# Optimization experiments

Measured on AMD Instinct MI355X. Metric: run time of the kernel, lower is better.

## Reference

```python
import jax, jax.numpy as jnp
import numpy as np

N, E, F_IN, EDGE_DIM, EMB, H, L, DENSE = 50000, 800000, 16, 4, 32, 4, 2, 128
HC = EMB * H


def setup_inputs() -> dict:
    ks = iter(jax.random.split(jax.random.key(0), 64))

    def w(shape, fan):
        return jax.random.normal(next(ks), shape, jnp.float32) / np.float32(np.sqrt(fan))

    inp = {}
    inp['x'] = jax.random.normal(next(ks), (N, F_IN), jnp.float32)
    inp['edge_index'] = jax.random.randint(next(ks), (2, E), 0, N, jnp.int32)
    inp['edge_attr'] = jax.random.normal(next(ks), (E, EDGE_DIM), jnp.float32)
    # layer-0 TransformerConv (F_IN -> EMB, H heads) + transf Linear
    inp['Wq0'] = w((F_IN, HC), F_IN); inp['bq0'] = w((HC,), HC)
    inp['Wk0'] = w((F_IN, HC), F_IN); inp['bk0'] = w((HC,), HC)
    inp['Wv0'] = w((F_IN, HC), F_IN); inp['bv0'] = w((HC,), HC)
    inp['We0'] = w((EDGE_DIM, HC), EDGE_DIM)
    inp['Ws0'] = w((F_IN, HC), F_IN); inp['bs0'] = w((HC,), HC)
    inp['Wt0'] = w((HC, EMB), HC); inp['bt0'] = w((EMB,), EMB)
    # stacked L inner layers (EMB -> EMB)
    inp['Wq'] = w((L, EMB, HC), EMB); inp['bq'] = w((L, HC), HC)
    inp['Wk'] = w((L, EMB, HC), EMB); inp['bk'] = w((L, HC), HC)
    inp['Wv'] = w((L, EMB, HC), EMB); inp['bv'] = w((L, HC), HC)
    inp['We'] = w((L, EDGE_DIM, HC), EDGE_DIM)
    inp['Ws'] = w((L, EMB, HC), EMB); inp['bs'] = w((L, HC), HC)
    inp['Wt'] = w((L, HC, EMB), HC); inp['bt'] = w((L, EMB), EMB)
    # dense head
    inp['W1'] = w((EMB, DENSE), EMB); inp['b1'] = w((DENSE,), DENSE)
    inp['W2'] = w((DENSE, DENSE // 2), DENSE); inp['b2'] = w((DENSE // 2,), DENSE)
    inp['W3'] = w((DENSE // 2, 1), DENSE // 2); inp['b3'] = w((1,), 1)
    return inp


def _tconv(h, edge_attr, src, dst, Wq, bq, Wk, bk, Wv, bv, We, Ws, bs):
    """PyG TransformerConv: edge-conditioned multi-head attention + root skip."""
    n = h.shape[0]
    q = (h @ Wq + bq).reshape(n, H, EMB)
    k = (h @ Wk + bk).reshape(n, H, EMB)
    v = (h @ Wv + bv).reshape(n, H, EMB)
    e = (edge_attr @ We).reshape(-1, H, EMB)          # [E,H,C]
    kj = k[src] + e                                   # gather + edge bias
    logits = (q[dst] * kj).sum(-1) / np.float32(np.sqrt(EMB))  # [E,H]
    m = jax.ops.segment_max(logits, dst, num_segments=n)       # segment softmax
    p = jnp.exp(logits - m[dst])
    z = jax.ops.segment_sum(p, dst, num_segments=n)
    alpha = p / (z[dst] + 1e-16)
    msg = (v[src] + e) * alpha[:, :, None]
    out = jax.ops.segment_sum(msg, dst, num_segments=n).reshape(n, HC)
    return out + h @ Ws + bs                          # root_weight skip


def _forward(x, edge_attr, Wq0, bq0, Wk0, bk0, Wv0, bv0, We0, Ws0, bs0, Wt0, bt0,
             Wq, bq, Wk, bk, Wv, bv, We, Ws, bs, Wt, bt,
             W1, b1, W2, b2, W3, b3, edge_index):
    src, dst = edge_index[0], edge_index[1]
    h = _tconv(x, edge_attr, src, dst, Wq0, bq0, Wk0, bk0, Wv0, bv0, We0, Ws0, bs0)
    h = jax.nn.relu(h @ Wt0 + bt0)
    for i in range(L):
        h = _tconv(h, edge_attr, src, dst, Wq[i], bq[i], Wk[i], bk[i],
                   Wv[i], bv[i], We[i], Ws[i], bs[i])
        h = jax.nn.relu(h @ Wt[i] + bt[i])
    h = jax.nn.relu(h @ W1 + b1)
    h = jax.nn.relu(h @ W2 + b2)
    return jax.nn.sigmoid(h @ W3 + b3)                # [N,1]


def reference(x, edge_index, edge_attr, Wq0, bq0, Wk0, bk0, Wv0, bv0, We0, Ws0, bs0,
              Wt0, bt0, Wq, bq, Wk, bk, Wv, bv, We, Ws, bs, Wt, bt,
              W1, b1, W2, b2, W3, b3):
    return _forward(x, edge_attr, Wq0, bq0, Wk0, bk0, Wv0, bv0, We0, Ws0, bs0,
                    Wt0, bt0, Wq, bq, Wk, bk, Wv, bv, We, Ws, bs, Wt, bt,
                    W1, b1, W2, b2, W3, b3, edge_index)
```

## Files before the change

### kernel.cpp

```cpp
#include <hip/hip_runtime.h>

#define NN 50000
#define EE 800000
#define FIN 16
#define EDIM 4
#define EMB 32
#define NH 4
#define HC 128
#define NL 2
#define DENSE 128
#define QNPB 50
#define SBLK 49

__device__ __forceinline__ float2 h2f2(unsigned int u) {
    union { unsigned int u; _Float16 h[2]; } c; c.u = u;
    return make_float2((float)c.h[0], (float)c.h[1]);
}

__global__ void hist_kernel(const int* __restrict__ dst, int* __restrict__ counts) {
    int e = blockIdx.x * blockDim.x + threadIdx.x;
    if (e < EE) atomicAdd(&counts[dst[e]], 1);
}

__global__ __launch_bounds__(1024) void scan1_kernel(const int* __restrict__ cursor,
                                                     int* __restrict__ row_ptr,
                                                     int* __restrict__ bsum) {
    __shared__ int wsum[16];
    __shared__ int wpre[17];
    int tid = threadIdx.x, lane = tid & 63, wid = tid >> 6;
    int i = blockIdx.x * 1024 + tid;
    int v = (i < NN) ? cursor[i] : 0;
    int incl = v;
    #pragma unroll
    for (int off = 1; off < 64; off <<= 1) {
        int t = __shfl_up(incl, off, 64);
        if (lane >= off) incl += t;
    }
    if (lane == 63) wsum[wid] = incl;
    __syncthreads();
    if (tid == 0) {
        int acc = 0;
        #pragma unroll
        for (int w = 0; w < 16; ++w) { wpre[w] = acc; acc += wsum[w]; }
        wpre[16] = acc;
    }
    __syncthreads();
    if (i < NN) row_ptr[i] = wpre[wid] + incl - v;
    if (tid == 0) bsum[blockIdx.x] = wpre[16];
}

__global__ void scan2_kernel(int* __restrict__ bsum, int* __restrict__ row_ptr) {
    int t = threadIdx.x;
    int v = (t < SBLK) ? bsum[t] : 0;
    int incl = v;
    #pragma unroll
    for (int off = 1; off < 64; off <<= 1) {
        int u = __shfl_up(incl, off, 64);
        if (t >= off) incl += u;
    }
    if (t < SBLK) bsum[t] = incl - v;
    if (t == 63) row_ptr[NN] = incl;
}

__global__ __launch_bounds__(1024) void scan3_kernel(int* __restrict__ row_ptr,
                                                     int* __restrict__ cursor,
                                                     const int* __restrict__ bsum) {
    int i = blockIdx.x * 1024 + threadIdx.x;
    if (i >= NN) return;
    int r = row_ptr[i] + bsum[blockIdx.x];
    row_ptr[i] = r;
    cursor[i] = r;
}

__global__ void scatter_kernel(const int* __restrict__ src, const int* __restrict__ dst,
                               const float* __restrict__ ea, int* __restrict__ cursor,
                               int* __restrict__ ssrc, float4* __restrict__ sea) {
    int e = blockIdx.x * blockDim.x + threadIdx.x;
    if (e >= EE) return;
    int d = dst[e];
    int pos = atomicAdd(&cursor[d], 1);
    ssrc[pos] = src[e];
    sea[pos] = *reinterpret_cast<const float4*>(ea + (size_t)e * 4);
}

__global__ __launch_bounds__(512) void qkvs0_kernel(const float* __restrict__ x,
        const float* __restrict__ Wq, const float* __restrict__ bq,
        const float* __restrict__ Wk, const float* __restrict__ bk,
        const float* __restrict__ Wv, const float* __restrict__ bv,
        const float* __restrict__ Ws, const float* __restrict__ bs,
        float* __restrict__ Q, _Float16* __restrict__ kvh,
        float* __restrict__ Out) {
    __shared__ float hs[QNPB][FIN];
    int tid = threadIdx.x;
    int m = tid >> 7, c = tid & 127;
    const float* W; const float* b;
    switch (m) {
        case 0:  W = Wq; b = bq; break;
        case 1:  W = Wk; b = bk; break;
        case 2:  W = Wv; b = bv; break;
        default: W = Ws; b = bs; break;
    }
    float w[FIN];
    #pragma unroll
    for (int f = 0; f < FIN; ++f) w[f] = W[f * HC + c];
    float bias = b[c];
    int node0 = blockIdx.x * QNPB;
    for (int i = tid; i < QNPB * FIN; i += 512)
        hs[i / FIN][i % FIN] = x[(size_t)node0 * FIN + i];
    __syncthreads();
    for (int k = 0; k < QNPB; ++k) {
        float s = bias;
        #pragma unroll
        for (int f = 0; f < FIN; ++f) s += hs[k][f] * w[f];
        size_t n = node0 + k;
        if      (m == 0) Q[n * HC + c] = s;
        else if (m == 1) kvh[n * 256 + 2 * c] = (_Float16)s;
        else if (m == 2) kvh[n * 256 + 2 * c + 1] = (_Float16)s;
        else             Out[n * HC + c] = s;
    }
}

__global__ __launch_bounds__(512) void ftq_kernel(const float* __restrict__ Wt,
        const float* __restrict__ bt,
        const float* __restrict__ Wq, const float* __restrict__ bq,
        const float* __restrict__ Wk, const float* __restrict__ bk,
        const float* __restrict__ Wv, const float* __restrict__ bv,
        const float* __restrict__ Ws, const float* __restrict__ bs,
        float* __restrict__ Q, _Float16* __restrict__ kvh,
        float* __restrict__ Out) {
    __shared__ float os[QNPB * HC];
    __shared__ float hs[QNPB][EMB];
    int tid = threadIdx.x;
    int node0 = blockIdx.x * QNPB;
    for (int i = tid; i < QNPB * HC; i += 512)
        os[i] = Out[(size_t)node0 * HC + i];
    __syncthreads();
    for (int idx = tid; idx < QNPB * EMB; idx += 512) {
        int nl = idx >> 5, c = idx & 31;
        float s = bt[c];
        const float* r = os + nl * HC;
        #pragma unroll 8
        for (int j = 0; j < HC; ++j) s += r[j] * Wt[j * EMB + c];
        hs[nl][c] = fmaxf(s, 0.f);
    }
    __syncthreads();
    int m = tid >> 7, c = tid & 127;
    const float* W; const float* b;
    switch (m) {
        case 0:  W = Wq; b = bq; break;
        case 1:  W = Wk; b = bk; break;
        case 2:  W = Wv; b = bv; break;
        default: W = Ws; b = bs; break;
    }
    float w[EMB];
    #pragma unroll
    for (int f = 0; f < EMB; ++f) w[f] = W[f * HC + c];
    float bias = b[c];
    for (int k = 0; k < QNPB; ++k) {
        float s = bias;
        #pragma unroll
        for (int f = 0; f < EMB; ++f) s += hs[k][f] * w[f];
        size_t n = node0 + k;
        if      (m == 0) Q[n * HC + c] = s;
        else if (m == 1) kvh[n * 256 + 2 * c] = (_Float16)s;
        else if (m == 2) kvh[n * 256 + 2 * c + 1] = (_Float16)s;
        else             Out[n * HC + c] = s;
    }
}

__global__ __launch_bounds__(256) void edge_attn_kernel(const int* __restrict__ row_ptr,
        const int* __restrict__ ssrc, const float4* __restrict__ sea,
        const float* __restrict__ We,
        const float* __restrict__ Q, const uint2* __restrict__ kvp,
        float2* __restrict__ Out) {
    int n = blockIdx.x * 4 + (threadIdx.x >> 6);
    int lane = threadIdx.x & 63;
    int ch0 = 2 * lane, ch1 = 2 * lane + 1;
    float we0[4], we1[4];
    #pragma unroll
    for (int d = 0; d < 4; ++d) { we0[d] = We[d * HC + ch0]; we1[d] = We[d * HC + ch1]; }
    float2 q = ((const float2*)Q)[(size_t)n * 64 + lane];
    int start = row_ptr[n], end = row_ptr[n + 1];
    float z = 0.f, acc0 = 0.f, acc1 = 0.f;
    const float SC = 0.17677669529663687f;
    int i = start;
    for (; i + 1 < end; i += 2) {
        int sA = ssrc[i], sB = ssrc[i + 1];
        sA = sA < 0 ? 0 : (sA >= NN ? NN - 1 : sA);
        sB = sB < 0 ? 0 : (sB >= NN ? NN - 1 : sB);
        float4 eA = sea[i], eB = sea[i + 1];
        uint2 kvA = kvp[(size_t)sA * 64 + lane];
        uint2 kvB = kvp[(size_t)sB * 64 + lane];
        float eA0 = eA.x * we0[0] + eA.y * we0[1] + eA.z * we0[2] + eA.w * we0[3];
        float eA1 = eA.x * we1[0] + eA.y * we1[1] + eA.z * we1[2] + eA.w * we1[3];
        float eB0 = eB.x * we0[0] + eB.y * we0[1] + eB.z * we0[2] + eB.w * we0[3];
        float eB1 = eB.x * we1[0] + eB.y * we1[1] + eB.z * we1[2] + eB.w * we1[3];
        float2 kvA0 = h2f2(kvA.x), kvA1 = h2f2(kvA.y);
        float2 kvB0 = h2f2(kvB.x), kvB1 = h2f2(kvB.y);
        float pA = q.x * (kvA0.x + eA0) + q.y * (kvA1.x + eA1);
        float pB = q.x * (kvB0.x + eB0) + q.y * (kvB1.x + eB1);
        #pragma unroll
        for (int off = 1; off < 16; off <<= 1) {
            pA += __shfl_xor(pA, off, 64);
            pB += __shfl_xor(pB, off, 64);
        }
        float xA = __expf(pA * SC), xB = __expf(pB * SC);
        z += xA + xB;
        acc0 += xA * (kvA0.y + eA0) + xB * (kvB0.y + eB0);
        acc1 += xA * (kvA1.y + eA1) + xB * (kvB1.y + eB1);
    }
    if (i < end) {
        int s = ssrc[i];
        s = s < 0 ? 0 : (s >= NN ? NN - 1 : s);
        float4 e = sea[i];
        uint2 kv = kvp[(size_t)s * 64 + lane];
        float e0 = e.x * we0[0] + e.y * we0[1] + e.z * we0[2] + e.w * we0[3];
        float e1 = e.x * we1[0] + e.y * we1[1] + e.z * we1[2] + e.w * we1[3];
        float2 kv0 = h2f2(kv.x), kv1 = h2f2(kv.y);
        float p = q.x * (kv0.x + e0) + q.y * (kv1.x + e1);
        #pragma unroll
        for (int off = 1; off < 16; off <<= 1) p += __shfl_xor(p, off, 64);
        float x = __expf(p * SC);
        z += x;
        acc0 += x * (kv0.y + e0);
        acc1 += x * (kv1.y + e1);
    }
    float inv = 1.f / (z + 1e-16f);
    size_t oi = (size_t)n * 64 + lane;
    float2 o = Out[oi];
    o.x += acc0 * inv;
    o.y += acc1 * inv;
    Out[oi] = o;
}

__global__ __launch_bounds__(512) void head2_kernel(const float* __restrict__ Outb,
        const float* __restrict__ Wt, const float* __restrict__ bt,
        const float* __restrict__ W1, const float* __restrict__ b1,
        const float* __restrict__ W2, const float* __restrict__ b2,
        const float* __restrict__ W3, const float* __restrict__ b3,
        float* __restrict__ out) {
    __shared__ float os[QNPB * HC];
    __shared__ float hs[QNPB * EMB];
    __shared__ float d2s[QNPB * 64];
    float* d1s = os;
    int tid = threadIdx.x;
    int node0 = blockIdx.x * QNPB;
    int g = tid >> 7;

    for (int i = tid; i < QNPB * HC; i += 512)
        os[i] = Outb[(size_t)node0 * HC + i];

    int cT = (tid & 127) >> 2, seg = tid & 3;
    float wt[32];
    #pragma unroll
    for (int j = 0; j < 32; ++j) wt[j] = Wt[(seg * 32 + j) * EMB + cT];
    float btc = bt[cT];
    __syncthreads();
    for (int k = g; k < QNPB; k += 4) {
        float p = 0.f;
        const float* r = os + k * HC + seg * 32;
        #pragma unroll
        for (int j = 0; j < 32; ++j) p += r[j] * wt[j];
        p += __shfl_xor(p, 1, 64);
        p += __shfl_xor(p, 2, 64);
        if (seg == 0) hs[k * EMB + cT] = fmaxf(p + btc, 0.f);
    }
    __syncthreads();

    int c1 = tid & 127;
    float w1[32];
    #pragma unroll
    for (int f = 0; f < 32; ++f) w1[f] = W1[f * DENSE + c1];
    float b1c = b1[c1];
    for (int k = g; k < QNPB; k += 4) {
        float s = b1c;
        #pragma unroll
        for (int f = 0; f < 32; ++f) s += hs[k * EMB + f] * w1[f];
        d1s[k * DENSE + c1] = fmaxf(s, 0.f);
    }
    __syncthreads();

    int c2 = (tid & 127) >> 1, hh = tid & 1;
    float w2[64];
    #pragma unroll
    for (int j = 0; j < 64; ++j) w2[j] = W2[(hh * 64 + j) * 64 + c2];
    float b2c = b2[c2];
    for (int k = g; k < QNPB; k += 4) {
        float p = 0.f;
        const float* r = d1s + k * DENSE + hh * 64;
        #pragma unroll
        for (int j = 0; j < 64; ++j) p += r[j] * w2[j];
        p += __shfl_xor(p, 1, 64);
        if (hh == 0) d2s[k * 64 + c2] = fmaxf(p + b2c, 0.f);
    }
    __syncthreads();

    int w = tid >> 6, lane = tid & 63;
    float w3r = W3[lane];
    float b3r = b3[0];
    for (int k = w; k < QNPB; k += 8) {
        float t = d2s[k * 64 + lane] * w3r;
        #pragma unroll
        for (int off = 1; off < 64; off <<= 1) t += __shfl_xor(t, off, 64);
        if (lane == 0) out[node0 + k] = 1.f / (1.f + __expf(-(t + b3r)));
    }
}

extern "C" void kernel_launch(void* const* d_in, const int* in_sizes, int n_in,
                              void* d_out, int out_size, void* d_ws, size_t ws_size,
                              hipStream_t stream) {
    const float* x   = (const float*)d_in[0];
    const int*   ei  = (const int*)d_in[1];
    const float* ea  = (const float*)d_in[2];
    const float* Wq0 = (const float*)d_in[3];  const float* bq0 = (const float*)d_in[4];
    const float* Wk0 = (const float*)d_in[5];  const float* bk0 = (const float*)d_in[6];
    const float* Wv0 = (const float*)d_in[7];  const float* bv0 = (const float*)d_in[8];
    const float* We0 = (const float*)d_in[9];
    const float* Ws0 = (const float*)d_in[10]; const float* bs0 = (const float*)d_in[11];
    const float* Wt0 = (const float*)d_in[12]; const float* bt0 = (const float*)d_in[13];
    const float* WqL = (const float*)d_in[14]; const float* bqL = (const float*)d_in[15];
    const float* WkL = (const float*)d_in[16]; const float* bkL = (const float*)d_in[17];
    const float* WvL = (const float*)d_in[18]; const float* bvL = (const float*)d_in[19];
    const float* WeL = (const float*)d_in[20];
    const float* WsL = (const float*)d_in[21]; const float* bsL = (const float*)d_in[22];
    const float* WtL = (const float*)d_in[23]; const float* btL = (const float*)d_in[24];
    const float* W1  = (const float*)d_in[25]; const float* b1  = (const float*)d_in[26];
    const float* W2  = (const float*)d_in[27]; const float* b2  = (const float*)d_in[28];
    const float* W3  = (const float*)d_in[29]; const float* b3  = (const float*)d_in[30];
    float* out = (float*)d_out;

    char* ws = (char*)d_ws;
    size_t off = 0;
    auto alloc = [&](size_t bytes) -> void* {
        void* p = ws + off; off = (off + bytes + 255) & ~(size_t)255; return p;
    };
    int*     cursor  = (int*)    alloc((size_t)NN * 4);
    int*     row_ptr = (int*)    alloc((size_t)(NN + 1) * 4);
    int*     bsum    = (int*)    alloc((size_t)SBLK * 4);
    int*     ssrc    = (int*)    alloc((size_t)EE * 4);
    float4*  sea     = (float4*) alloc((size_t)EE * 16);
    float*   Q       = (float*)  alloc((size_t)NN * HC * 4);
    _Float16* kvh    = (_Float16*)alloc((size_t)NN * HC * 2 * 2);
    float*   Outb    = (float*)  alloc((size_t)NN * HC * 4);

    hipMemsetAsync(cursor, 0, (size_t)NN * 4, stream);
    hist_kernel<<<(EE + 255) / 256, 256, 0, stream>>>(ei + EE, cursor);
    scan1_kernel<<<SBLK, 1024, 0, stream>>>(cursor, row_ptr, bsum);
    scan2_kernel<<<1, 64, 0, stream>>>(bsum, row_ptr);
    scan3_kernel<<<SBLK, 1024, 0, stream>>>(row_ptr, cursor, bsum);
    scatter_kernel<<<(EE + 255) / 256, 256, 0, stream>>>(ei, ei + EE, ea, cursor, ssrc, sea);

    const uint2* kvp = (const uint2*)kvh;
    float2* Out2 = (float2*)Outb;

    qkvs0_kernel<<<NN / QNPB, 512, 0, stream>>>(x, Wq0, bq0, Wk0, bk0, Wv0, bv0,
                                                Ws0, bs0, Q, kvh, Outb);
    edge_attn_kernel<<<NN / 4, 256, 0, stream>>>(row_ptr, ssrc, sea, We0, Q, kvp, Out2);

    ftq_kernel<<<NN / QNPB, 512, 0, stream>>>(Wt0, bt0,
        WqL, bqL, WkL, bkL, WvL, bvL, WsL, bsL, Q, kvh, Outb);
    edge_attn_kernel<<<NN / 4, 256, 0, stream>>>(row_ptr, ssrc, sea, WeL, Q, kvp, Out2);

    ftq_kernel<<<NN / QNPB, 512, 0, stream>>>(WtL, btL,
        WqL + EMB * HC, bqL + HC, WkL + EMB * HC, bkL + HC,
        WvL + EMB * HC, bvL + HC, WsL + EMB * HC, bsL + HC, Q, kvh, Outb);
    edge_attn_kernel<<<NN / 4, 256, 0, stream>>>(row_ptr, ssrc, sea,
        WeL + EDIM * HC, Q, kvp, Out2);

    head2_kernel<<<NN / QNPB, 512, 0, stream>>>(Outb, WtL + (size_t)HC * EMB, btL + EMB,
                                                W1, b1, W2, b2, W3, b3, out);
}
```

Measured before the change: 652.3 us.

## Factor edge-embedding projection out of attention loop and parallelize Wt transform

The edge attention kernel now precomputes, per head, the projection of the query onto the edge-weight columns. Logits get the edge term as a 4-term dot with the raw edge attributes, and the value-side edge contribution is accumulated as four weighted attribute sums that are multiplied by We once at the end. This removes the per-edge, per-channel edge-embedding math from the hot loop. Separately, the fused transform kernel splits the 128-wide Wt dot product across four lanes with weights held in registers and combines them with shuffles, which adds register pressure.

After: 669.6 us. +2.7%, slower.

```diff
diff --git a/kernel.cpp b/kernel.cpp
--- a/kernel.cpp
+++ b/kernel.cpp
@@ -129,21 +129,31 @@
         float* __restrict__ Q, _Float16* __restrict__ kvh,
         float* __restrict__ Out) {
     __shared__ float os[QNPB * HC];
-    __shared__ float hs[QNPB][EMB];
+    __shared__ float hs[QNPB * EMB];
     int tid = threadIdx.x;
     int node0 = blockIdx.x * QNPB;
+    int g = tid >> 7;
+
     for (int i = tid; i < QNPB * HC; i += 512)
         os[i] = Out[(size_t)node0 * HC + i];
-    __syncthreads();
-    for (int idx = tid; idx < QNPB * EMB; idx += 512) {
-        int nl = idx >> 5, c = idx & 31;
-        float s = bt[c];
-        const float* r = os + nl * HC;
-        #pragma unroll 8
-        for (int j = 0; j < HC; ++j) s += r[j] * Wt[j * EMB + c];
-        hs[nl][c] = fmaxf(s, 0.f);
-    }
-    __syncthreads();
+
+    int cT = (tid & 127) >> 2, seg = tid & 3;
+    float wt[32];
+    #pragma unroll
+    for (int j = 0; j < 32; ++j) wt[j] = Wt[(seg * 32 + j) * EMB + cT];
+    float btc = bt[cT];
+    __syncthreads();
+    for (int k = g; k < QNPB; k += 4) {
+        float p = 0.f;
+        const float* r = os + k * HC + seg * 32;
+        #pragma unroll
+        for (int j = 0; j < 32; ++j) p += r[j] * wt[j];
+        p += __shfl_xor(p, 1, 64);
+        p += __shfl_xor(p, 2, 64);
+        if (seg == 0) hs[k * EMB + cT] = fmaxf(p + btc, 0.f);
+    }
+    __syncthreads();
+
     int m = tid >> 7, c = tid & 127;
     const float* W; const float* b;
     switch (m) {
@@ -159,7 +169,7 @@
     for (int k = 0; k < QNPB; ++k) {
         float s = bias;
         #pragma unroll
-        for (int f = 0; f < EMB; ++f) s += hs[k][f] * w[f];
+        for (int f = 0; f < EMB; ++f) s += hs[k * EMB + f] * w[f];
         size_t n = node0 + k;
         if      (m == 0) Q[n * HC + c] = s;
         else if (m == 1) kvh[n * 256 + 2 * c] = (_Float16)s;
@@ -180,8 +190,17 @@
     #pragma unroll
     for (int d = 0; d < 4; ++d) { we0[d] = We[d * HC + ch0]; we1[d] = We[d * HC + ch1]; }
     float2 q = ((const float2*)Q)[(size_t)n * 64 + lane];
+    float u[4];
+    #pragma unroll
+    for (int d = 0; d < 4; ++d) {
+        float t = q.x * we0[d] + q.y * we1[d];
+        #pragma unroll
+        for (int off = 1; off < 16; off <<= 1) t += __shfl_xor(t, off, 64);
+        u[d] = t;
+    }
     int start = row_ptr[n], end = row_ptr[n + 1];
     float z = 0.f, acc0 = 0.f, acc1 = 0.f;
+    float g0 = 0.f, g1 = 0.f, g2 = 0.f, g3 = 0.f;
     const float SC = 0.17677669529663687f;
     int i = start;
     for (; i + 1 < end; i += 2) {
@@ -191,45 +210,47 @@
         float4 eA = sea[i], eB = sea[i + 1];
         uint2 kvA = kvp[(size_t)sA * 64 + lane];
         uint2 kvB = kvp[(size_t)sB * 64 + lane];
-        float eA0 = eA.x * we0[0] + eA.y * we0[1] + eA.z * we0[2] + eA.w * we0[3];
-        float eA1 = eA.x * we1[0] + eA.y * we1[1] + eA.z * we1[2] + eA.w * we1[3];
-        float eB0 = eB.x * we0[0] + eB.y * we0[1] + eB.z * we0[2] + eB.w * we0[3];
-        float eB1 = eB.x * we1[0] + eB.y * we1[1] + eB.z * we1[2] + eB.w * we1[3];
-        float2 kvA0 = h2f2(kvA.x), kvA1 = h2f2(kvA.y);
-        float2 kvB0 = h2f2(kvB.x), kvB1 = h2f2(kvB.y);
-        float pA = q.x * (kvA0.x + eA0) + q.y * (kvA1.x + eA1);
-        float pB = q.x * (kvB0.x + eB0) + q.y * (kvB1.x + eB1);
+        float2 kA0 = h2f2(kvA.x), kA1 = h2f2(kvA.y);
+        float2 kB0 = h2f2(kvB.x), kB1 = h2f2(kvB.y);
+        float pA = q.x * kA0.x + q.y * kA1.x;
+        float pB = q.x * kB0.x + q.y * kB1.x;
         #pragma unroll
         for (int off = 1; off < 16; off <<= 1) {
             pA += __shfl_xor(pA, off, 64);
             pB += __shfl_xor(pB, off, 64);
         }
+        pA += u[0] * eA.x + u[1] * eA.y + u[2] * eA.z + u[3] * eA.w;
+        pB += u[0] * eB.x + u[1] * eB.y + u[2] * eB.z + u[3] * eB.w;
         float xA = __expf(pA * SC), xB = __expf(pB * SC);
         z += xA + xB;
-        acc0 += xA * (kvA0.y + eA0) + xB * (kvB0.y + eB0);
-        acc1 += xA * (kvA1.y + eA1) + xB * (kvB1.y + eB1);
+        acc0 += xA * kA0.y + xB * kB0.y;
+        acc1 += xA * kA1.y + xB * kB1.y;
+        g0 += xA * eA.x + xB * eB.x;
+        g1 += xA * eA.y + xB * eB.y;
+        g2 += xA * eA.z + xB * eB.z;
+        g3 += xA * eA.w + xB * eB.w;
     }
     if (i < end) {
         int s = ssrc[i];
         s = s < 0 ? 0 : (s >= NN ? NN - 1 : s);
         float4 e = sea[i];
         uint2 kv = kvp[(size_t)s * 64 + lane];
-        float e0 = e.x * we0[0] + e.y * we0[1] + e.z * we0[2] + e.w * we0[3];
-        float e1 = e.x * we1[0] + e.y * we1[1] + e.z * we1[2] + e.w * we1[3];
-        float2 kv0 = h2f2(kv.x), kv1 = h2f2(kv.y);
-        float p = q.x * (kv0.x + e0) + q.y * (kv1.x + e1);
+        float2 k0 = h2f2(kv.x), k1 = h2f2(kv.y);
+        float p = q.x * k0.x + q.y * k1.x;
         #pragma unroll
         for (int off = 1; off < 16; off <<= 1) p += __shfl_xor(p, off, 64);
+        p += u[0] * e.x + u[1] * e.y + u[2] * e.z + u[3] * e.w;
         float x = __expf(p * SC);
         z += x;
-        acc0 += x * (kv0.y + e0);
-        acc1 += x * (kv1.y + e1);
+        acc0 += x * k0.y;
+        acc1 += x * k1.y;
+        g0 += x * e.x; g1 += x * e.y; g2 += x * e.z; g3 += x * e.w;
     }
     float inv = 1.f / (z + 1e-16f);
     size_t oi = (size_t)n * 64 + lane;
     float2 o = Out[oi];
-    o.x += acc0 * inv;
-    o.y += acc1 * inv;
+    o.x += (acc0 + g0 * we0[0] + g1 * we0[1] + g2 * we0[2] + g3 * we0[3]) * inv;
+    o.y += (acc1 + g0 * we1[0] + g1 * we1[1] + g2 * we1[2] + g3 * we1[3]) * inv;
     Out[oi] = o;
 }
 
```

## Vectorize shared-memory loads and restructure ftq Wt projection with register weights

Applied to the files above, without the earlier changes.

Global-to-shared copies and shared-memory row reads in qkvs0, ftq and head2 now use float4, which cuts the number of LDS and global load instructions. The ftq kernel's Wt projection changes from per-thread streaming of Wt from global memory to the head2 scheme: each thread keeps 32 Wt weights in registers and the partial sums are combined with shuffles across 4 lanes. This removes repeated global weight reads in the node-transform step. It also changes the order of floating-point summation and raises register pressure.

Measured after the change: 637.4 us. -2.3%, faster.

```diff
diff --git a/kernel.cpp b/kernel.cpp
--- a/kernel.cpp
+++ b/kernel.cpp
@@ -90,7 +90,7 @@
         const float* __restrict__ Ws, const float* __restrict__ bs,
         float* __restrict__ Q, _Float16* __restrict__ kvh,
         float* __restrict__ Out) {
-    __shared__ float hs[QNPB][FIN];
+    __shared__ __align__(16) float hs[QNPB * FIN];
     int tid = threadIdx.x;
     int m = tid >> 7, c = tid & 127;
     const float* W; const float* b;
@@ -105,13 +105,21 @@
     for (int f = 0; f < FIN; ++f) w[f] = W[f * HC + c];
     float bias = b[c];
     int node0 = blockIdx.x * QNPB;
-    for (int i = tid; i < QNPB * FIN; i += 512)
-        hs[i / FIN][i % FIN] = x[(size_t)node0 * FIN + i];
-    __syncthreads();
+    {
+        const float4* src4 = (const float4*)(x + (size_t)node0 * FIN);
+        float4* dst4 = (float4*)hs;
+        for (int i = tid; i < QNPB * FIN / 4; i += 512) dst4[i] = src4[i];
+    }
+    __syncthreads();
+    const float4* hs4 = (const float4*)hs;
     for (int k = 0; k < QNPB; ++k) {
         float s = bias;
         #pragma unroll
-        for (int f = 0; f < FIN; ++f) s += hs[k][f] * w[f];
+        for (int f4 = 0; f4 < FIN / 4; ++f4) {
+            float4 hv = hs4[k * (FIN / 4) + f4];
+            s += hv.x * w[4 * f4] + hv.y * w[4 * f4 + 1]
+               + hv.z * w[4 * f4 + 2] + hv.w * w[4 * f4 + 3];
+        }
         size_t n = node0 + k;
         if      (m == 0) Q[n * HC + c] = s;
         else if (m == 1) kvh[n * 256 + 2 * c] = (_Float16)s;
@@ -128,22 +136,39 @@
         const float* __restrict__ Ws, const float* __restrict__ bs,
         float* __restrict__ Q, _Float16* __restrict__ kvh,
         float* __restrict__ Out) {
-    __shared__ float os[QNPB * HC];
-    __shared__ float hs[QNPB][EMB];
+    __shared__ __align__(16) float os[QNPB * HC];
+    __shared__ __align__(16) float hs[QNPB * EMB];
     int tid = threadIdx.x;
     int node0 = blockIdx.x * QNPB;
-    for (int i = tid; i < QNPB * HC; i += 512)
-        os[i] = Out[(size_t)node0 * HC + i];
-    __syncthreads();
-    for (int idx = tid; idx < QNPB * EMB; idx += 512) {
-        int nl = idx >> 5, c = idx & 31;
-        float s = bt[c];
-        const float* r = os + nl * HC;
-        #pragma unroll 8
-        for (int j = 0; j < HC; ++j) s += r[j] * Wt[j * EMB + c];
-        hs[nl][c] = fmaxf(s, 0.f);
-    }
-    __syncthreads();
+    int g = tid >> 7;
+
+    {
+        const float4* src4 = (const float4*)(Out + (size_t)node0 * HC);
+        float4* dst4 = (float4*)os;
+        for (int i = tid; i < QNPB * HC / 4; i += 512) dst4[i] = src4[i];
+    }
+
+    int cT = (tid & 127) >> 2, seg = tid & 3;
+    float wt[32];
+    #pragma unroll
+    for (int j = 0; j < 32; ++j) wt[j] = Wt[(seg * 32 + j) * EMB + cT];
+    float btc = bt[cT];
+    __syncthreads();
+    for (int k = g; k < QNPB; k += 4) {
+        float p = 0.f;
+        const float4* r4 = (const float4*)(os + k * HC + seg * 32);
+        #pragma unroll
+        for (int j4 = 0; j4 < 8; ++j4) {
+            float4 rv = r4[j4];
+            p += rv.x * wt[4 * j4] + rv.y * wt[4 * j4 + 1]
+               + rv.z * wt[4 * j4 + 2] + rv.w * wt[4 * j4 + 3];
+        }
+        p += __shfl_xor(p, 1, 64);
+        p += __shfl_xor(p, 2, 64);
+        if (seg == 0) hs[k * EMB + cT] = fmaxf(p + btc, 0.f);
+    }
+    __syncthreads();
+
     int m = tid >> 7, c = tid & 127;
     const float* W; const float* b;
     switch (m) {
@@ -156,10 +181,15 @@
     #pragma unroll
     for (int f = 0; f < EMB; ++f) w[f] = W[f * HC + c];
     float bias = b[c];
+    const float4* hs4 = (const float4*)hs;
     for (int k = 0; k < QNPB; ++k) {
         float s = bias;
         #pragma unroll
-        for (int f = 0; f < EMB; ++f) s += hs[k][f] * w[f];
+        for (int f4 = 0; f4 < EMB / 4; ++f4) {
+            float4 hv = hs4[k * (EMB / 4) + f4];
+            s += hv.x * w[4 * f4] + hv.y * w[4 * f4 + 1]
+               + hv.z * w[4 * f4 + 2] + hv.w * w[4 * f4 + 3];
+        }
         size_t n = node0 + k;
         if      (m == 0) Q[n * HC + c] = s;
         else if (m == 1) kvh[n * 256 + 2 * c] = (_Float16)s;
@@ -239,16 +269,19 @@
         const float* __restrict__ W2, const float* __restrict__ b2,
         const float* __restrict__ W3, const float* __restrict__ b3,
         float* __restrict__ out) {
-    __shared__ float os[QNPB * HC];
-    __shared__ float hs[QNPB * EMB];
-    __shared__ float d2s[QNPB * 64];
+    __shared__ __align__(16) float os[QNPB * HC];
+    __shared__ __align__(16) float hs[QNPB * EMB];
+    __shared__ __align__(16) float d2s[QNPB * 64];
     float* d1s = os;
     int tid = threadIdx.x;
     int node0 = blockIdx.x * QNPB;
     int g = tid >> 7;
 
-    for (int i = tid; i < QNPB * HC; i += 512)
-        os[i] = Outb[(size_t)node0 * HC + i];
+    {
+        const float4* src4 = (const float4*)(Outb + (size_t)node0 * HC);
+        float4* dst4 = (float4*)os;
+        for (int i = tid; i < QNPB * HC / 4; i += 512) dst4[i] = src4[i];
+    }
 
     int cT = (tid & 127) >> 2, seg = tid & 3;
     float wt[32];
@@ -258,9 +291,13 @@
     __syncthreads();
     for (int k = g; k < QNPB; k += 4) {
         float p = 0.f;
-        const float* r = os + k * HC + seg * 32;
-        #pragma unroll
-        for (int j = 0; j < 32; ++j) p += r[j] * wt[j];
+        const float4* r4 = (const float4*)(os + k * HC + seg * 32);
+        #pragma unroll
+        for (int j4 = 0; j4 < 8; ++j4) {
+            float4 rv = r4[j4];
+            p += rv.x * wt[4 * j4] + rv.y * wt[4 * j4 + 1]
+               + rv.z * wt[4 * j4 + 2] + rv.w * wt[4 * j4 + 3];
+        }
         p += __shfl_xor(p, 1, 64);
         p += __shfl_xor(p, 2, 64);
         if (seg == 0) hs[k * EMB + cT] = fmaxf(p + btc, 0.f);
@@ -272,10 +309,15 @@
     #pragma unroll
     for (int f = 0; f < 32; ++f) w1[f] = W1[f * DENSE + c1];
     float b1c = b1[c1];
+    const float4* hs4 = (const float4*)hs;
     for (int k = g; k < QNPB; k += 4) {
         float s = b1c;
         #pragma unroll
-        for (int f = 0; f < 32; ++f) s += hs[k * EMB + f] * w1[f];
+        for (int f4 = 0; f4 < 8; ++f4) {
+            float4 hv = hs4[k * 8 + f4];
+            s += hv.x * w1[4 * f4] + hv.y * w1[4 * f4 + 1]
+               + hv.z * w1[4 * f4 + 2] + hv.w * w1[4 * f4 + 3];
+        }
         d1s[k * DENSE + c1] = fmaxf(s, 0.f);
     }
     __syncthreads();
@@ -287,9 +329,13 @@
     float b2c = b2[c2];
     for (int k = g; k < QNPB; k += 4) {
         float p = 0.f;
-        const float* r = d1s + k * DENSE + hh * 64;
-        #pragma unroll
-        for (int j = 0; j < 64; ++j) p += r[j] * w2[j];
+        const float4* r4 = (const float4*)(d1s + k * DENSE + hh * 64);
+        #pragma unroll
+        for (int j4 = 0; j4 < 16; ++j4) {
+            float4 rv = r4[j4];
+            p += rv.x * w2[4 * j4] + rv.y * w2[4 * j4 + 1]
+               + rv.z * w2[4 * j4 + 2] + rv.w * w2[4 * j4 + 3];
+        }
         p += __shfl_xor(p, 1, 64);
         if (hh == 0) d2s[k * 64 + c2] = fmaxf(p + b2c, 0.f);
     }
```
